# Optimization experiments

Hardware: AMD Instinct MI355X
Metric: run time of the kernel (lower is better)

## Reference

```python
import jax, jax.numpy as jnp
import numpy as np


def _gcn_conv(x, W, b, src, dst, dinv):
    # PyG GCNConv: linear transform, then symmetric-normalized aggregation, then bias
    n = x.shape[0]
    h = x @ W  # [N, out]
    norm = (dinv[src] * dinv[dst])[:, None]  # [E, 1]
    msg = h[src] * norm  # gather + scale, [E, out]
    out = jax.ops.segment_sum(msg, dst, num_segments=n)  # scatter-add
    return out + b


def setup_inputs() -> dict:
    key = jax.random.key(0)
    k1, k2, k3, k4 = jax.random.split(key, 4)
    N, E, F_IN, F_HID, F_OUT = 50000, 800000, 512, 256, 64
    x = jax.random.normal(k1, (N, F_IN), dtype=jnp.float32)
    edge_index = jax.random.randint(k2, (2, E), 0, N, dtype=jnp.int64)
    # Glorot-ish init for weights
    W1 = jax.random.normal(k3, (F_IN, F_HID), dtype=jnp.float32) * (1.0 / np.sqrt(F_IN))
    b1 = jnp.zeros((F_HID,), dtype=jnp.float32)
    W2 = jax.random.normal(k4, (F_HID, F_OUT), dtype=jnp.float32) * (1.0 / np.sqrt(F_HID))
    b2 = jnp.zeros((F_OUT,), dtype=jnp.float32)
    return {"x": x, "edge_index": edge_index, "W1": W1, "b1": b1, "W2": W2, "b2": b2}


def reference(x, edge_index, W1, b1, W2, b2):
    n = x.shape[0]
    # Add self loops (GCNConv default)
    loop = jnp.arange(n, dtype=edge_index.dtype)
    src = jnp.concatenate([edge_index[0], loop])
    dst = jnp.concatenate([edge_index[1], loop])
    # Symmetric normalization D^{-1/2} (A+I) D^{-1/2}
    deg = jax.ops.segment_sum(jnp.ones_like(dst, dtype=x.dtype), dst, num_segments=n)
    dinv = jnp.where(deg > 0, jax.lax.rsqrt(deg), 0.0)
    h = _gcn_conv(x, W1, b1, src, dst, dinv)
    h = jax.nn.relu(h)
    # Dropout(p=0.5) is identity in eval mode (deterministic reference)
    h = _gcn_conv(h, W2, b2, src, dst, dinv)
    return jax.nn.log_softmax(h, axis=1)
```

## Files before the change

### kernel.cpp

```cpp
#include <hip/hip_runtime.h>
#include <math.h>

#define F_IN  512
#define F_HID 256
#define F_OUT 64

typedef __attribute__((ext_vector_type(8))) short bf16x8;
typedef __attribute__((ext_vector_type(4))) short bf16x4;
typedef __attribute__((ext_vector_type(4))) float f32x4;

#define GLOBAL_AS __attribute__((address_space(1)))
#define LDS_AS    __attribute__((address_space(3)))

__device__ __forceinline__ void gload_lds16(const ushort* g, ushort* l) {
    __builtin_amdgcn_global_load_lds((const GLOBAL_AS uint32_t*)g,
                                     (LDS_AS uint32_t*)l, 16, 0, 0);
}

__device__ __forceinline__ ushort f2bf(float f) {
    union { float f; uint32_t u; } v; v.f = f;
    uint32_t r = (v.u + 0x7FFFu + ((v.u >> 16) & 1u)) >> 16;
    return (ushort)r;
}

__device__ __forceinline__ float bf2f(ushort u) {
    union { uint32_t u; float f; } v; v.u = ((uint32_t)u) << 16;
    return v.f;
}

__global__ void k_deg(const int* __restrict__ dst, int* __restrict__ deg, int E) {
    int e = blockIdx.x * 256 + threadIdx.x;
    if (e < E) atomicAdd(&deg[dst[e]], 1);
}

__global__ void k_dinv(const int* __restrict__ deg, float* __restrict__ dinv, int N) {
    int i = blockIdx.x * 256 + threadIdx.x;
    if (i < N) dinv[i] = rsqrtf((float)(deg[i] + 1));
}

__global__ void k_scan1(const int* __restrict__ deg, int* __restrict__ offs,
                        int* __restrict__ bsums, int N) {
    __shared__ int s[256];
    int tid = threadIdx.x;
    int i = blockIdx.x * 256 + tid;
    int v = (i < N) ? deg[i] : 0;
    s[tid] = v; __syncthreads();
    for (int d = 1; d < 256; d <<= 1) {
        int t = (tid >= d) ? s[tid - d] : 0;
        __syncthreads();
        s[tid] += t;
        __syncthreads();
    }
    if (i < N) offs[i] = s[tid] - v;
    if (tid == 255) bsums[blockIdx.x] = s[255];
}

__global__ void k_scan2(int* __restrict__ bsums, int n) {
    __shared__ int s[256];
    int tid = threadIdx.x;
    int v = (tid < n) ? bsums[tid] : 0;
    s[tid] = v; __syncthreads();
    for (int d = 1; d < 256; d <<= 1) {
        int t = (tid >= d) ? s[tid - d] : 0;
        __syncthreads();
        s[tid] += t;
        __syncthreads();
    }
    if (tid < n) bsums[tid] = s[tid] - v;
}

__global__ void k_scan3(int* __restrict__ offs, const int* __restrict__ bsums,
                        int* __restrict__ cursor, int2* __restrict__ jw, int N, int E) {
    int i = blockIdx.x * 256 + threadIdx.x;
    if (i < N) {
        int o = offs[i] + bsums[i >> 8];
        offs[i] = o;
        cursor[i] = o;
    }
    if (i == 0) offs[N] = E;
    if (i < 8) jw[E + i] = make_int2(0, 0);
}

__global__ void k_fill(const int* __restrict__ src, const int* __restrict__ dst,
                       int* __restrict__ cursor, int2* __restrict__ jw,
                       const float* __restrict__ dinv, int E) {
    int e = blockIdx.x * 256 + threadIdx.x;
    if (e < E) {
        int s = src[e];
        int pos = atomicAdd(&cursor[dst[e]], 1);
        jw[pos] = make_int2(s, __float_as_int(dinv[s]));
    }
}

__global__ void k_cast_bf16(const float* __restrict__ in, ushort* __restrict__ outp, int n8) {
    int i = blockIdx.x * 256 + threadIdx.x;
    if (i >= n8) return;
    const float4* p = (const float4*)in + (size_t)i * 2;
    float4 v0 = p[0], v1 = p[1];
    bf16x8 o;
    o[0] = (short)f2bf(v0.x); o[1] = (short)f2bf(v0.y);
    o[2] = (short)f2bf(v0.z); o[3] = (short)f2bf(v0.w);
    o[4] = (short)f2bf(v1.x); o[5] = (short)f2bf(v1.y);
    o[6] = (short)f2bf(v1.z); o[7] = (short)f2bf(v1.w);
    *(bf16x8*)&outp[(size_t)i * 8] = o;
}

__global__ void k_tcast(const float* __restrict__ in, ushort* __restrict__ outp, int K, int Nc) {
    int idx = blockIdx.x * 256 + threadIdx.x;
    if (idx >= K * Nc) return;
    int n = idx / K, k = idx - n * K;
    outp[idx] = f2bf(in[(size_t)k * Nc + n]);
}

template<int WR, int WC, int MR, int NR, bool OUT_BF16>
__global__ __launch_bounds__(256) void k_gemm_bf16(
        const ushort* __restrict__ A, const ushort* __restrict__ Bt,
        void* __restrict__ Cv, int M, int K, int Nc) {
    constexpr int BM = WR * MR * 16;
    constexpr int BN = WC * NR * 16;
    __shared__ ushort As[BM * 32];
    __shared__ ushort Bs[BN * 32];
    const int tid  = threadIdx.x;
    const int wave = tid >> 6, lane = tid & 63;
    const int wr = wave % WR, wc = wave / WR;
    const int brow = blockIdx.y * BM, bcol = blockIdx.x * BN;

    f32x4 acc[MR][NR];
    #pragma unroll
    for (int m = 0; m < MR; ++m)
        #pragma unroll
        for (int n = 0; n < NR; ++n) acc[m][n] = (f32x4){0.f, 0.f, 0.f, 0.f};

    const int srow = tid >> 2;
    const int scol = (tid & 3) * 8;
    const int kq  = (lane >> 4) * 8;
    const int rA0 = wr * MR * 16 + (lane & 15);
    const int rB0 = wc * NR * 16 + (lane & 15);

    for (int k0 = 0; k0 < K; k0 += 32) {
        #pragma unroll
        for (int l = 0; l < BM / 64; ++l) {
            int row = brow + l * 64 + srow;
            if (row >= M) row = M - 1;
            gload_lds16(&A[(size_t)row * K + k0 + scol], &As[l * 2048 + wave * 512]);
        }
        #pragma unroll
        for (int l = 0; l < BN / 64; ++l) {
            int row = bcol + l * 64 + srow;
            gload_lds16(&Bt[(size_t)row * K + k0 + scol], &Bs[l * 2048 + wave * 512]);
        }
        __syncthreads();
        bf16x8 af[MR], bfr[NR];
        #pragma unroll
        for (int m = 0; m < MR; ++m)
            af[m] = *(const bf16x8*)&As[(rA0 + m * 16) * 32 + kq];
        #pragma unroll
        for (int n = 0; n < NR; ++n)
            bfr[n] = *(const bf16x8*)&Bs[(rB0 + n * 16) * 32 + kq];
        #pragma unroll
        for (int m = 0; m < MR; ++m)
            #pragma unroll
            for (int n = 0; n < NR; ++n)
                acc[m][n] = __builtin_amdgcn_mfma_f32_16x16x32_bf16(af[m], bfr[n], acc[m][n], 0, 0, 0);
        __syncthreads();
    }

    const int crow0 = brow + wr * MR * 16 + (lane >> 4) * 4;
    const int ccol0 = bcol + wc * NR * 16 + (lane & 15);
    #pragma unroll
    for (int m = 0; m < MR; ++m)
        #pragma unroll
        for (int n = 0; n < NR; ++n)
            #pragma unroll
            for (int j = 0; j < 4; ++j) {
                int row = crow0 + m * 16 + j;
                if (row < M) {
                    if constexpr (OUT_BF16)
                        ((ushort*)Cv)[(size_t)row * Nc + ccol0 + n * 16] = f2bf(acc[m][n][j]);
                    else
                        ((float*)Cv)[(size_t)row * Nc + ccol0 + n * 16] = acc[m][n][j];
                }
            }
}

__global__ __launch_bounds__(256) void k_agg1(
        const ushort* __restrict__ h, const int2* __restrict__ jw,
        const int* __restrict__ offs, const float* __restrict__ dinv,
        const float* __restrict__ bias, ushort* __restrict__ outm, int N) {
    int wave = threadIdx.x >> 6, lane = threadIdx.x & 63;
    int i = blockIdx.x * 4 + wave;
    if (i >= N) return;
    float di = dinv[i];
    float acc0, acc1, acc2, acc3;
    {
        bf16x4 hv = *(const bf16x4*)&h[(size_t)i * F_HID + lane * 4];
        float w = di * di;
        acc0 = bf2f((ushort)hv[0]) * w; acc1 = bf2f((ushort)hv[1]) * w;
        acc2 = bf2f((ushort)hv[2]) * w; acc3 = bf2f((ushort)hv[3]) * w;
    }
    int s = offs[i], e = offs[i + 1];
    for (int u = s; u < e; u += 8) {
        int2 a[8];
        #pragma unroll
        for (int q = 0; q < 8; ++q) a[q] = jw[u + q];
        bf16x4 hv[8];
        #pragma unroll
        for (int q = 0; q < 8; ++q)
            hv[q] = *(const bf16x4*)&h[(size_t)a[q].x * F_HID + lane * 4];
        #pragma unroll
        for (int q = 0; q < 8; ++q) {
            float ww = (u + q < e) ? __int_as_float(a[q].y) * di : 0.f;
            acc0 += bf2f((ushort)hv[q][0]) * ww;
            acc1 += bf2f((ushort)hv[q][1]) * ww;
            acc2 += bf2f((ushort)hv[q][2]) * ww;
            acc3 += bf2f((ushort)hv[q][3]) * ww;
        }
    }
    const float4* bp = (const float4*)&bias[lane * 4];
    float4 bv = *bp;
    bf16x4 o;
    o[0] = (short)f2bf(fmaxf(acc0 + bv.x, 0.f));
    o[1] = (short)f2bf(fmaxf(acc1 + bv.y, 0.f));
    o[2] = (short)f2bf(fmaxf(acc2 + bv.z, 0.f));
    o[3] = (short)f2bf(fmaxf(acc3 + bv.w, 0.f));
    *(bf16x4*)&outm[(size_t)i * F_HID + lane * 4] = o;
}

__global__ __launch_bounds__(256) void k_agg2(
        const ushort* __restrict__ h, const int2* __restrict__ jw,
        const int* __restrict__ offs, const float* __restrict__ dinv,
        const float* __restrict__ bias, float* __restrict__ outm, int N) {
    int wave = threadIdx.x >> 6, lane = threadIdx.x & 63;
    int i = blockIdx.x * 4 + wave;
    if (i >= N) return;
    float di = dinv[i];
    float acc = bf2f(h[(size_t)i * F_OUT + lane]) * di * di;
    int s = offs[i], e = offs[i + 1];
    for (int u = s; u < e; u += 8) {
        int2 a[8];
        #pragma unroll
        for (int q = 0; q < 8; ++q) a[q] = jw[u + q];
        float hv[8];
        #pragma unroll
        for (int q = 0; q < 8; ++q)
            hv[q] = bf2f(h[(size_t)a[q].x * F_OUT + lane]);
        #pragma unroll
        for (int q = 0; q < 8; ++q) {
            float ww = (u + q < e) ? __int_as_float(a[q].y) * di : 0.f;
            acc += hv[q] * ww;
        }
    }
    acc += bias[lane];
    float m = acc;
    #pragma unroll
    for (int o = 32; o >= 1; o >>= 1) m = fmaxf(m, __shfl_xor(m, o, 64));
    float ex = expf(acc - m);
    float ssum = ex;
    #pragma unroll
    for (int o = 32; o >= 1; o >>= 1) ssum += __shfl_xor(ssum, o, 64);
    outm[(size_t)i * F_OUT + lane] = acc - m - logf(ssum);
}

extern "C" void kernel_launch(void* const* d_in, const int* in_sizes, int n_in,
                              void* d_out, int out_size, void* d_ws, size_t ws_size,
                              hipStream_t stream) {
    const float* x  = (const float*)d_in[0];
    const int*   ei = (const int*)d_in[1];
    const float* W1 = (const float*)d_in[2];
    const float* b1 = (const float*)d_in[3];
    const float* W2 = (const float*)d_in[4];
    const float* b2 = (const float*)d_in[5];
    float* out = (float*)d_out;

    int N = in_sizes[0] / F_IN;
    int E = in_sizes[1] / 2;
    const int* src = ei;
    const int* dst = ei + E;

    ushort* xb  = (ushort*)d_ws;
    ushort* w1t = xb + (size_t)N * F_IN;
    ushort* w2t = w1t + F_HID * F_IN;
    ushort* h1  = w2t + F_OUT * F_HID;
    int*    deg = (int*)(h1 + (size_t)N * F_HID);
    float*  dinv = (float*)(deg + N);
    int*    offs = (int*)(dinv + N);
    int*    cursor = offs + N + 1;
    int*    bsums  = cursor + N;
    int2*   jw     = (int2*)(bsums + 256 + 1);
    jw = (int2*)(((uintptr_t)(bsums + 256) + 7) & ~(uintptr_t)7);
    ushort* a1b = xb;
    ushort* h2  = h1;

    int nch = (N + 255) / 256;

    hipMemsetAsync(deg, 0, sizeof(int) * N, stream);
    k_deg <<<(E + 255) / 256, 256, 0, stream>>>(dst, deg, E);
    k_dinv<<<(N + 255) / 256, 256, 0, stream>>>(deg, dinv, N);
    k_scan1<<<nch, 256, 0, stream>>>(deg, offs, bsums, N);
    k_scan2<<<1, 256, 0, stream>>>(bsums, nch);
    k_scan3<<<nch, 256, 0, stream>>>(offs, bsums, cursor, jw, N, E);
    k_fill<<<(E + 255) / 256, 256, 0, stream>>>(src, dst, cursor, jw, dinv, E);

    int n8 = N * F_IN / 8;
    k_cast_bf16<<<(n8 + 255) / 256, 256, 0, stream>>>(x, xb, n8);
    k_tcast<<<(F_IN * F_HID + 255) / 256, 256, 0, stream>>>(W1, w1t, F_IN, F_HID);
    k_tcast<<<(F_HID * F_OUT + 255) / 256, 256, 0, stream>>>(W2, w2t, F_HID, F_OUT);

    k_gemm_bf16<2, 2, 4, 4, true><<<dim3(F_HID / 128, (N + 127) / 128), 256, 0, stream>>>(
        xb, w1t, (void*)h1, N, F_IN, F_HID);
    k_agg1<<<(N + 3) / 4, 256, 0, stream>>>(h1, jw, offs, dinv, b1, a1b, N);

    k_gemm_bf16<4, 1, 2, 4, true><<<dim3(F_OUT / 64, (N + 127) / 128), 256, 0, stream>>>(
        a1b, w2t, (void*)h2, N, F_HID, F_OUT);
    k_agg2<<<(N + 3) / 4, 256, 0, stream>>>(h2, jw, offs, dinv, b2, out, N);
}
```

Baseline: 265.0 us.

## Fuse x cast into GEMM1, merge small kernels, widen aggregation loads

```diff
diff --git a/kernel.cpp b/kernel.cpp
--- a/kernel.cpp
+++ b/kernel.cpp
@@ -33,17 +33,13 @@
     if (e < E) atomicAdd(&deg[dst[e]], 1);
 }
 
-__global__ void k_dinv(const int* __restrict__ deg, float* __restrict__ dinv, int N) {
-    int i = blockIdx.x * 256 + threadIdx.x;
-    if (i < N) dinv[i] = rsqrtf((float)(deg[i] + 1));
-}
-
 __global__ void k_scan1(const int* __restrict__ deg, int* __restrict__ offs,
-                        int* __restrict__ bsums, int N) {
+                        int* __restrict__ bsums, float* __restrict__ dinv, int N) {
     __shared__ int s[256];
     int tid = threadIdx.x;
     int i = blockIdx.x * 256 + tid;
     int v = (i < N) ? deg[i] : 0;
+    if (i < N) dinv[i] = rsqrtf((float)(v + 1));
     s[tid] = v; __syncthreads();
     for (int d = 1; d < 256; d <<= 1) {
         int t = (tid >= d) ? s[tid - d] : 0;
@@ -78,7 +74,7 @@
         cursor[i] = o;
     }
     if (i == 0) offs[N] = E;
-    if (i < 8) jw[E + i] = make_int2(0, 0);
+    if (i < 16) jw[E + i] = make_int2(0, 0);
 }
 
 __global__ void k_fill(const int* __restrict__ src, const int* __restrict__ dst,
@@ -92,30 +88,98 @@
     }
 }
 
-__global__ void k_cast_bf16(const float* __restrict__ in, ushort* __restrict__ outp, int n8) {
-    int i = blockIdx.x * 256 + threadIdx.x;
-    if (i >= n8) return;
-    const float4* p = (const float4*)in + (size_t)i * 2;
-    float4 v0 = p[0], v1 = p[1];
-    bf16x8 o;
-    o[0] = (short)f2bf(v0.x); o[1] = (short)f2bf(v0.y);
-    o[2] = (short)f2bf(v0.z); o[3] = (short)f2bf(v0.w);
-    o[4] = (short)f2bf(v1.x); o[5] = (short)f2bf(v1.y);
-    o[6] = (short)f2bf(v1.z); o[7] = (short)f2bf(v1.w);
-    *(bf16x8*)&outp[(size_t)i * 8] = o;
-}
-
-__global__ void k_tcast(const float* __restrict__ in, ushort* __restrict__ outp, int K, int Nc) {
+__global__ void k_tcast2(const float* __restrict__ W1, ushort* __restrict__ w1t,
+                         const float* __restrict__ W2, ushort* __restrict__ w2t) {
     int idx = blockIdx.x * 256 + threadIdx.x;
-    if (idx >= K * Nc) return;
-    int n = idx / K, k = idx - n * K;
-    outp[idx] = f2bf(in[(size_t)k * Nc + n]);
-}
-
-template<int WR, int WC, int MR, int NR, bool OUT_BF16>
+    const int n1 = F_IN * F_HID;
+    if (idx < n1) {
+        int n = idx / F_IN, k = idx - n * F_IN;
+        w1t[idx] = f2bf(W1[(size_t)k * F_HID + n]);
+    } else {
+        int t = idx - n1;
+        if (t < F_HID * F_OUT) {
+            int n = t / F_HID, k = t - n * F_HID;
+            w2t[t] = f2bf(W2[(size_t)k * F_OUT + n]);
+        }
+    }
+}
+
+__global__ __launch_bounds__(256) void k_gemm1_fused(
+        const float* __restrict__ A, const ushort* __restrict__ Bt,
+        ushort* __restrict__ C, int M) {
+    constexpr int K = F_IN, Nc = F_HID, BM = 64;
+    constexpr int ASTR = 40;
+    constexpr int BCH = 257 * 8;
+    __shared__ ushort As[BM * ASTR];
+    __shared__ ushort Bs[4 * BCH];
+    const int tid  = threadIdx.x;
+    const int wave = tid >> 6, lane = tid & 63;
+    const int brow = blockIdx.x * BM;
+
+    f32x4 acc[4][4];
+    #pragma unroll
+    for (int m = 0; m < 4; ++m)
+        #pragma unroll
+        for (int n = 0; n < 4; ++n) acc[m][n] = (f32x4){0.f, 0.f, 0.f, 0.f};
+
+    const int arow = tid >> 2;
+    const int akc  = (tid & 3) * 8;
+    int agrow = brow + arow; if (agrow >= M) agrow = M - 1;
+    const float* aptr = &A[(size_t)agrow * K + akc];
+
+    const int kq  = (lane >> 4) * 8;
+    const int rA0 = lane & 15;
+    const int cF  = wave * 64 + (lane & 15);
+
+    for (int k0 = 0; k0 < K; k0 += 32) {
+        float4 v0 = *(const float4*)(aptr + k0);
+        float4 v1 = *(const float4*)(aptr + k0 + 4);
+        bf16x8 av;
+        av[0] = (short)f2bf(v0.x); av[1] = (short)f2bf(v0.y);
+        av[2] = (short)f2bf(v0.z); av[3] = (short)f2bf(v0.w);
+        av[4] = (short)f2bf(v1.x); av[5] = (short)f2bf(v1.y);
+        av[6] = (short)f2bf(v1.z); av[7] = (short)f2bf(v1.w);
+        *(bf16x8*)&As[arow * ASTR + akc] = av;
+        #pragma unroll
+        for (int l = 0; l < 4; ++l) {
+            int m_ = wave * 4 + l;
+            int c = m_ & 3, rg = m_ >> 2;
+            gload_lds16(&Bt[(size_t)(rg * 64 + lane) * K + k0 + c * 8],
+                        &Bs[c * BCH + rg * 64 * 8]);
+        }
+        __syncthreads();
+        bf16x8 af[4], bfr[4];
+        #pragma unroll
+        for (int m = 0; m < 4; ++m)
+            af[m] = *(const bf16x8*)&As[(rA0 + m * 16) * ASTR + kq];
+        #pragma unroll
+        for (int n = 0; n < 4; ++n)
+            bfr[n] = *(const bf16x8*)&Bs[(lane >> 4) * BCH + (cF + n * 16) * 8];
+        #pragma unroll
+        for (int m = 0; m < 4; ++m)
+            #pragma unroll
+            for (int n = 0; n < 4; ++n)
+                acc[m][n] = __builtin_amdgcn_mfma_f32_16x16x32_bf16(af[m], bfr[n], acc[m][n], 0, 0, 0);
+        __syncthreads();
+    }
+
+    const int crow0 = brow + (lane >> 4) * 4;
+    const int ccol0 = wave * 64 + (lane & 15);
+    #pragma unroll
+    for (int m = 0; m < 4; ++m)
+        #pragma unroll
+        for (int n = 0; n < 4; ++n)
+            #pragma unroll
+            for (int j = 0; j < 4; ++j) {
+                int row = crow0 + m * 16 + j;
+                if (row < M) C[(size_t)row * Nc + ccol0 + n * 16] = f2bf(acc[m][n][j]);
+            }
+}
+
+template<int WR, int WC, int MR, int NR>
 __global__ __launch_bounds__(256) void k_gemm_bf16(
         const ushort* __restrict__ A, const ushort* __restrict__ Bt,
-        void* __restrict__ Cv, int M, int K, int Nc) {
+        ushort* __restrict__ C, int M, int K, int Nc) {
     constexpr int BM = WR * MR * 16;
     constexpr int BN = WC * NR * 16;
     __shared__ ushort As[BM * 32];
@@ -174,12 +238,7 @@
             #pragma unroll
             for (int j = 0; j < 4; ++j) {
                 int row = crow0 + m * 16 + j;
-                if (row < M) {
-                    if constexpr (OUT_BF16)
-                        ((ushort*)Cv)[(size_t)row * Nc + ccol0 + n * 16] = f2bf(acc[m][n][j]);
-                    else
-                        ((float*)Cv)[(size_t)row * Nc + ccol0 + n * 16] = acc[m][n][j];
-                }
+                if (row < M) C[(size_t)row * Nc + ccol0 + n * 16] = f2bf(acc[m][n][j]);
             }
 }
 
@@ -190,40 +249,48 @@
     int wave = threadIdx.x >> 6, lane = threadIdx.x & 63;
     int i = blockIdx.x * 4 + wave;
     if (i >= N) return;
+    int g = lane & 31;
+    int p = lane >> 5;
     float di = dinv[i];
-    float acc0, acc1, acc2, acc3;
+    float acc[8];
     {
-        bf16x4 hv = *(const bf16x4*)&h[(size_t)i * F_HID + lane * 4];
-        float w = di * di;
-        acc0 = bf2f((ushort)hv[0]) * w; acc1 = bf2f((ushort)hv[1]) * w;
-        acc2 = bf2f((ushort)hv[2]) * w; acc3 = bf2f((ushort)hv[3]) * w;
+        bf16x8 hv = *(const bf16x8*)&h[(size_t)i * F_HID + g * 8];
+        float w = (p == 0) ? di * di : 0.f;
+        #pragma unroll
+        for (int k = 0; k < 8; ++k) acc[k] = bf2f((ushort)hv[k]) * w;
     }
     int s = offs[i], e = offs[i + 1];
-    for (int u = s; u < e; u += 8) {
-        int2 a[8];
-        #pragma unroll
-        for (int q = 0; q < 8; ++q) a[q] = jw[u + q];
-        bf16x4 hv[8];
-        #pragma unroll
-        for (int q = 0; q < 8; ++q)
-            hv[q] = *(const bf16x4*)&h[(size_t)a[q].x * F_HID + lane * 4];
-        #pragma unroll
-        for (int q = 0; q < 8; ++q) {
-            float ww = (u + q < e) ? __int_as_float(a[q].y) * di : 0.f;
-            acc0 += bf2f((ushort)hv[q][0]) * ww;
-            acc1 += bf2f((ushort)hv[q][1]) * ww;
-            acc2 += bf2f((ushort)hv[q][2]) * ww;
-            acc3 += bf2f((ushort)hv[q][3]) * ww;
-        }
-    }
-    const float4* bp = (const float4*)&bias[lane * 4];
-    float4 bv = *bp;
-    bf16x4 o;
-    o[0] = (short)f2bf(fmaxf(acc0 + bv.x, 0.f));
-    o[1] = (short)f2bf(fmaxf(acc1 + bv.y, 0.f));
-    o[2] = (short)f2bf(fmaxf(acc2 + bv.z, 0.f));
-    o[3] = (short)f2bf(fmaxf(acc3 + bv.w, 0.f));
-    *(bf16x4*)&outm[(size_t)i * F_HID + lane * 4] = o;
+    for (int u = s; u < e; u += 12) {
+        int2 a[6];
+        #pragma unroll
+        for (int q = 0; q < 6; ++q) a[q] = jw[u + 2 * q + p];
+        bf16x8 hv[6];
+        #pragma unroll
+        for (int q = 0; q < 6; ++q)
+            hv[q] = *(const bf16x8*)&h[(size_t)a[q].x * F_HID + g * 8];
+        #pragma unroll
+        for (int q = 0; q < 6; ++q) {
+            float ww = (u + 2 * q + p < e) ? __int_as_float(a[q].y) * di : 0.f;
+            #pragma unroll
+            for (int k = 0; k < 8; ++k) acc[k] += bf2f((ushort)hv[q][k]) * ww;
+        }
+    }
+    #pragma unroll
+    for (int k = 0; k < 8; ++k) acc[k] += __shfl_xor(acc[k], 32, 64);
+    if (p == 0) {
+        float4 b0 = *(const float4*)&bias[g * 8];
+        float4 b1 = *(const float4*)&bias[g * 8 + 4];
+        bf16x8 o;
+        o[0] = (short)f2bf(fmaxf(acc[0] + b0.x, 0.f));
+        o[1] = (short)f2bf(fmaxf(acc[1] + b0.y, 0.f));
+        o[2] = (short)f2bf(fmaxf(acc[2] + b0.z, 0.f));
+        o[3] = (short)f2bf(fmaxf(acc[3] + b0.w, 0.f));
+        o[4] = (short)f2bf(fmaxf(acc[4] + b1.x, 0.f));
+        o[5] = (short)f2bf(fmaxf(acc[5] + b1.y, 0.f));
+        o[6] = (short)f2bf(fmaxf(acc[6] + b1.z, 0.f));
+        o[7] = (short)f2bf(fmaxf(acc[7] + b1.w, 0.f));
+        *(bf16x8*)&outm[(size_t)i * F_HID + g * 8] = o;
+    }
 }
 
 __global__ __launch_bounds__(256) void k_agg2(
@@ -236,16 +303,16 @@
     float di = dinv[i];
     float acc = bf2f(h[(size_t)i * F_OUT + lane]) * di * di;
     int s = offs[i], e = offs[i + 1];
-    for (int u = s; u < e; u += 8) {
-        int2 a[8];
-        #pragma unroll
-        for (int q = 0; q < 8; ++q) a[q] = jw[u + q];
-        float hv[8];
-        #pragma unroll
-        for (int q = 0; q < 8; ++q)
+    for (int u = s; u < e; u += 16) {
+        int2 a[16];
+        #pragma unroll
+        for (int q = 0; q < 16; ++q) a[q] = jw[u + q];
+        float hv[16];
+        #pragma unroll
+        for (int q = 0; q < 16; ++q)
             hv[q] = bf2f(h[(size_t)a[q].x * F_OUT + lane]);
         #pragma unroll
-        for (int q = 0; q < 8; ++q) {
+        for (int q = 0; q < 16; ++q) {
             float ww = (u + q < e) ? __int_as_float(a[q].y) * di : 0.f;
             acc += hv[q] * ww;
         }
@@ -277,40 +344,34 @@
     const int* src = ei;
     const int* dst = ei + E;
 
-    ushort* xb  = (ushort*)d_ws;
-    ushort* w1t = xb + (size_t)N * F_IN;
+    ushort* w1t = (ushort*)d_ws;
     ushort* w2t = w1t + F_HID * F_IN;
     ushort* h1  = w2t + F_OUT * F_HID;
-    int*    deg = (int*)(h1 + (size_t)N * F_HID);
+    ushort* a1  = h1 + (size_t)N * F_HID;
+    int*    deg = (int*)(a1 + (size_t)N * F_HID);
     float*  dinv = (float*)(deg + N);
     int*    offs = (int*)(dinv + N);
     int*    cursor = offs + N + 1;
     int*    bsums  = cursor + N;
-    int2*   jw     = (int2*)(bsums + 256 + 1);
-    jw = (int2*)(((uintptr_t)(bsums + 256) + 7) & ~(uintptr_t)7);
-    ushort* a1b = xb;
-    ushort* h2  = h1;
+    int2*   jw = (int2*)(((uintptr_t)(bsums + 256) + 7) & ~(uintptr_t)7);
+    ushort* h2 = h1;
 
     int nch = (N + 255) / 256;
 
     hipMemsetAsync(deg, 0, sizeof(int) * N, stream);
     k_deg <<<(E + 255) / 256, 256, 0, stream>>>(dst, deg, E);
-    k_dinv<<<(N + 255) / 256, 256, 0, stream>>>(deg, dinv, N);
-    k_scan1<<<nch, 256, 0, stream>>>(deg, offs, bsums, N);
+    k_scan1<<<nch, 256, 0, stream>>>(deg, offs, bsums, dinv, N);
     k_scan2<<<1, 256, 0, stream>>>(bsums, nch);
     k_scan3<<<nch, 256, 0, stream>>>(offs, bsums, cursor, jw, N, E);
     k_fill<<<(E + 255) / 256, 256, 0, stream>>>(src, dst, cursor, jw, dinv, E);
 
-    int n8 = N * F_IN / 8;
-    k_cast_bf16<<<(n8 + 255) / 256, 256, 0, stream>>>(x, xb, n8);
-    k_tcast<<<(F_IN * F_HID + 255) / 256, 256, 0, stream>>>(W1, w1t, F_IN, F_HID);
-    k_tcast<<<(F_HID * F_OUT + 255) / 256, 256, 0, stream>>>(W2, w2t, F_HID, F_OUT);
-
-    k_gemm_bf16<2, 2, 4, 4, true><<<dim3(F_HID / 128, (N + 127) / 128), 256, 0, stream>>>(
-        xb, w1t, (void*)h1, N, F_IN, F_HID);
-    k_agg1<<<(N + 3) / 4, 256, 0, stream>>>(h1, jw, offs, dinv, b1, a1b, N);
-
-    k_gemm_bf16<4, 1, 2, 4, true><<<dim3(F_OUT / 64, (N + 127) / 128), 256, 0, stream>>>(
-        a1b, w2t, (void*)h2, N, F_HID, F_OUT);
+    int ntc = F_IN * F_HID + F_HID * F_OUT;
+    k_tcast2<<<(ntc + 255) / 256, 256, 0, stream>>>(W1, w1t, W2, w2t);
+
+    k_gemm1_fused<<<(N + 63) / 64, 256, 0, stream>>>(x, w1t, h1, N);
+    k_agg1<<<(N + 3) / 4, 256, 0, stream>>>(h1, jw, offs, dinv, b1, a1, N);
+
+    k_gemm_bf16<4, 1, 2, 4><<<dim3(1, (N + 127) / 128), 256, 0, stream>>>(
+        a1, w2t, h2, N, F_HID, F_OUT);
     k_agg2<<<(N + 3) / 4, 256, 0, stream>>>(h2, jw, offs, dinv, b2, out, N);
 }
```

After: 284.6 us. +7.4%, slower.
